# Performance work log

Hardware: AMD Instinct MI355X
Metric: run time of the kernel (lower is better)

## Reference

```python
import jax, jax.numpy as jnp
import numpy as np

B, N, C_IN = 8, 16384, 64
NPOINTS = 1024     # S: number of sampled centers (FPS)
NNEI = 32          # K: neighbors per center (ball query cap)
RADIUS = 0.2
EPS = 1e-5


def fps(pos, S):
    """Farthest point sampling, deterministic start at index 0. pos: [B,N,3] -> [B,S] int32."""
    b, n, _ = pos.shape

    def step(carry, _):
        dist, far = carry
        centroid = jnp.take_along_axis(pos, far[:, None, None], axis=1)  # [B,1,3]
        d = jnp.sum((pos - centroid) ** 2, axis=-1)                       # [B,N]
        dist = jnp.minimum(dist, d)
        return (dist, jnp.argmax(dist, axis=-1).astype(jnp.int32)), far

    init = (jnp.full((b, n), 1e10, pos.dtype), jnp.zeros((b,), jnp.int32))
    _, cent = jax.lax.scan(step, init, None, length=S)  # [S,B]
    return cent.T                                        # [B,S]


def gather(points, idx):
    """points [B,N,C], idx [B,...] -> [B,...,C] (per-batch fancy gather)."""
    return jax.vmap(lambda p, i: p[i])(points, idx)


def ball_query(pos, centers, radius, k):
    """Fixed-radius neighbor search. pos [B,N,3], centers [B,S,3] -> idx [B,S,K] int32.
    Pads short neighborhoods with the first in-radius point (the center itself)."""
    n = pos.shape[1]
    sqr = jnp.sum((centers[:, :, None, :] - pos[:, None, :, :]) ** 2, axis=-1)  # [B,S,N]
    idx = jnp.where(sqr <= radius * radius, jnp.arange(n, dtype=jnp.int32), n)
    idx = jnp.sort(idx, axis=-1)[..., :k]                                        # [B,S,K]
    first = idx[..., :1]
    return jnp.where(idx == n, first, idx)


def conv_bn_relu(x, w, b, g, be):
    """1x1 Conv2d + BatchNorm2d(training stats) + ReLU over grouped tensor x [B,S,K,Cin]."""
    h = jnp.einsum('bskc,cd->bskd', x, w) + b
    mu = jnp.mean(h, axis=(0, 1, 2), keepdims=True)
    var = jnp.mean((h - mu) ** 2, axis=(0, 1, 2), keepdims=True)
    h = (h - mu) * jax.lax.rsqrt(var + EPS) * g + be
    return jax.nn.relu(h)


def reference(pos, feat,
              w_sem1, b_sem1, g_sem1, be_sem1, w_sem2, b_sem2, g_sem2, be_sem2,
              w_geo1, b_geo1, g_geo1, be_geo1, w_geo2, b_geo2, g_geo2, be_geo2):
    centroids = fps(pos, NPOINTS)                       # [B,S]
    centers = gather(pos, centroids)                    # [B,S,3]
    idx = ball_query(pos, centers, RADIUS, NNEI)        # [B,S,K]

    grouped_pos = gather(pos, idx)                      # [B,S,K,3]
    grouped_feat = gather(feat, idx)                    # [B,S,K,C]
    center_rep = jnp.broadcast_to(centers[:, :, None, :], grouped_pos.shape)
    geo_in = jnp.concatenate([center_rep, grouped_pos], axis=-1)  # [B,S,K,6]

    h = conv_bn_relu(grouped_feat, w_sem1, b_sem1, g_sem1, be_sem1)
    h = conv_bn_relu(h, w_sem2, b_sem2, g_sem2, be_sem2)
    h_sem = jnp.max(h, axis=2)                          # [B,S,Cout] max-pool over neighbors

    hg = conv_bn_relu(geo_in, w_geo1, b_geo1, g_geo1, be_geo1)
    hg = conv_bn_relu(hg, w_geo2, b_geo2, g_geo2, be_geo2)
    h_geo = jnp.max(hg, axis=2)                         # [B,S,Cout]

    # original concatenates semantic and geo node features along dim 0
    return jnp.concatenate([h_sem, h_geo], axis=0)      # [2B,S,Cout]


def setup_inputs() -> dict:
    key = jax.random.key(0)
    ks = jax.random.split(key, 12)
    d = {
        'pos': jax.random.uniform(ks[0], (B, N, 3), jnp.float32),
        'feat': jax.random.normal(ks[1], (B, N, C_IN), jnp.float32),
        'w_sem1': jax.random.normal(ks[2], (64, 64), jnp.float32) * 0.05,
        'b_sem1': jnp.zeros((64,), jnp.float32),
        'g_sem1': jnp.ones((64,), jnp.float32),
        'be_sem1': jnp.zeros((64,), jnp.float32),
        'w_sem2': jax.random.normal(ks[3], (64, 128), jnp.float32) * 0.05,
        'b_sem2': jnp.zeros((128,), jnp.float32),
        'g_sem2': jnp.ones((128,), jnp.float32),
        'be_sem2': jnp.zeros((128,), jnp.float32),
        'w_geo1': jax.random.normal(ks[4], (6, 64), jnp.float32) * 0.05,
        'b_geo1': jnp.zeros((64,), jnp.float32),
        'g_geo1': jnp.ones((64,), jnp.float32),
        'be_geo1': jnp.zeros((64,), jnp.float32),
        'w_geo2': jax.random.normal(ks[5], (64, 128), jnp.float32) * 0.05,
        'b_geo2': jnp.zeros((128,), jnp.float32),
        'g_geo2': jnp.ones((128,), jnp.float32),
        'be_geo2': jnp.zeros((128,), jnp.float32),
    }
    return d
```

## Files before the change

### kernel.cpp

```cpp
#include <hip/hip_runtime.h>

#define NB 8
#define NPTS 16384
#define S 1024
#define KNEI 32
#define MROWS (NB*S*KNEI)

typedef float v2f __attribute__((ext_vector_type(2)));

#define DPP_MAXF0(CTRL, v) do {                                               \
    int _o = __builtin_amdgcn_update_dpp(0, __float_as_int(v),                \
                                         (CTRL), 0xF, 0xF, true);             \
    (v) = fmaxf((v), __int_as_float(_o));                                     \
  } while (0)

#define DPP_MINI(CTRL, v) do {                                                \
    int _o = __builtin_amdgcn_update_dpp((int)0x7fffffff, (v),                \
                                         (CTRL), 0xF, 0xF, false);            \
    (v) = (_o < (v)) ? _o : (v);                                              \
  } while (0)

#define DPP_MAXK0(CTRL, k) do {                                               \
    int _olo = __builtin_amdgcn_update_dpp(0, (int)(unsigned)(k),             \
                                           (CTRL), 0xF, 0xF, true);           \
    int _ohi = __builtin_amdgcn_update_dpp(0, (int)(unsigned)((k) >> 32),     \
                                           (CTRL), 0xF, 0xF, true);           \
    unsigned long long _ok = (((unsigned long long)(unsigned)_ohi) << 32)     \
                           | (unsigned)_olo;                                  \
    if (_ok > (k)) (k) = _ok;                                                 \
  } while (0)

#define DPP_ROW_SHR1   0x111
#define DPP_ROW_SHR2   0x112
#define DPP_ROW_SHR4   0x114
#define DPP_ROW_SHR8   0x118
#define DPP_ROW_BCAST15 0x142
#define DPP_ROW_BCAST31 0x143

__global__ __launch_bounds__(1024, 4) void fps_kernel(const float* __restrict__ pos,
                                                      float* __restrict__ centers,
                                                      float* __restrict__ sbuf){
#pragma clang fp contract(off)
  __shared__ int hist[4096];
  __shared__ int ts[1024];
  __shared__ unsigned short perm[16384];
  __shared__ unsigned long long lslotK[2][16];
  const int b = blockIdx.x;
  const int t = threadIdx.x;
  const int wid = t >> 6, lane = t & 63;
  const float* pb = pos + (size_t)b * NPTS * 3;
  float* ssx = sbuf + (size_t)b * 3 * NPTS;
  float* ssy = ssx + NPTS;
  float* ssz = ssy + NPTS;
  const int p0 = t * 16;

  float c[48];
  {
    const float4* src = (const float4*)(pb + (size_t)t*48);
#pragma unroll
    for (int q = 0; q < 12; ++q) *(float4*)&c[q*4] = src[q];
  }
  int cell[16];
#pragma unroll
  for (int j = 0; j < 16; ++j){
    float x = c[3*j], y = c[3*j+1], z = c[3*j+2];
    int ix = (int)(x * 16.f); ix = ix < 0 ? 0 : (ix > 15 ? 15 : ix);
    int iy = (int)(y * 16.f); iy = iy < 0 ? 0 : (iy > 15 ? 15 : iy);
    int iz = (int)(z * 16.f); iz = iz < 0 ? 0 : (iz > 15 ? 15 : iz);
    int m = 0;
#pragma unroll
    for (int k = 0; k < 4; ++k){
      m |= ((ix >> k) & 1) << (3*k + 2);
      m |= ((iy >> k) & 1) << (3*k + 1);
      m |= ((iz >> k) & 1) << (3*k + 0);
    }
    cell[j] = m;
  }
#pragma unroll
  for (int i = 0; i < 4; ++i) hist[t*4 + i] = 0;
  __syncthreads();
#pragma unroll
  for (int j = 0; j < 16; ++j) atomicAdd(&hist[cell[j]], 1);
  __syncthreads();
  int h0 = hist[t*4], h1 = hist[t*4+1], h2v = hist[t*4+2];
  ts[t] = h0 + h1 + h2v + hist[t*4+3];
  __syncthreads();
  for (int off = 1; off < 1024; off <<= 1){
    int add = (t >= off) ? ts[t - off] : 0;
    __syncthreads();
    ts[t] += add;
    __syncthreads();
  }
  {
    int base = (t == 0) ? 0 : ts[t-1];
    hist[t*4]   = base;
    hist[t*4+1] = base + h0;
    hist[t*4+2] = base + h0 + h1;
    hist[t*4+3] = base + h0 + h1 + h2v;
  }
  __syncthreads();
#pragma unroll
  for (int j = 0; j < 16; ++j){
    int dst = atomicAdd(&hist[cell[j]], 1);
    ssx[dst] = c[3*j];
    ssy[dst] = c[3*j+1];
    ssz[dst] = c[3*j+2];
    perm[dst] = (unsigned short)(p0 + j);
  }
  __syncthreads();

  v2f px[8], py[8], pz[8], dist[8];
  int perm_reg[8];
#pragma unroll
  for (int g = 0; g < 4; ++g){
    float4 vx = *(const float4*)&ssx[p0 + g*4];
    float4 vy = *(const float4*)&ssy[p0 + g*4];
    float4 vz = *(const float4*)&ssz[p0 + g*4];
    px[g*2]   = (v2f){vx.x, vx.y}; px[g*2+1] = (v2f){vx.z, vx.w};
    py[g*2]   = (v2f){vy.x, vy.y}; py[g*2+1] = (v2f){vy.z, vy.w};
    pz[g*2]   = (v2f){vz.x, vz.y}; pz[g*2+1] = (v2f){vz.z, vz.w};
  }
#pragma unroll
  for (int j = 0; j < 8; ++j){
    perm_reg[j] = (int)perm[p0 + 2*j] | ((int)perm[p0 + 2*j + 1] << 16);
  }
  float bxl = 1e30f, bxh = -1e30f, byl = 1e30f, byh = -1e30f;
  float bzl = 1e30f, bzh = -1e30f;
#pragma unroll
  for (int j = 0; j < 8; ++j){
    asm volatile("" : "+v"(px[j]), "+v"(py[j]), "+v"(pz[j]), "+v"(perm_reg[j]));
    bxl = fminf(bxl, fminf(px[j].x, px[j].y));
    bxh = fmaxf(bxh, fmaxf(px[j].x, px[j].y));
    byl = fminf(byl, fminf(py[j].x, py[j].y));
    byh = fmaxf(byh, fmaxf(py[j].x, py[j].y));
    bzl = fminf(bzl, fminf(pz[j].x, pz[j].y));
    bzh = fmaxf(bzh, fmaxf(pz[j].x, pz[j].y));
    dist[j] = (v2f){1e10f, 1e10f};
  }
  float ub = 1e10f;
  unsigned long long key = 0;
  float cx = pb[0], cy = pb[1], cz = pb[2];

  for (int s = 0; s < S; ++s){
    if (t == 0){
      float* cd = centers + (size_t)(b*S + s)*3;
      cd[0] = cx; cd[1] = cy; cd[2] = cz;
    }
    float lx = fmaxf(fmaxf(bxl - cx, cx - bxh), 0.f);
    float ly = fmaxf(fmaxf(byl - cy, cy - byh), 0.f);
    float lz = fmaxf(fmaxf(bzl - cz, cz - bzh), 0.f);
    float lb2 = ((lx*lx + ly*ly) + lz*lz);
    bool act = !(lb2 * 0.99999f >= ub);
    unsigned long long am = __ballot((int)act);
    if (am){
      if (act){
        v2f cx2 = (v2f){cx, cx}, cy2 = (v2f){cy, cy}, cz2 = (v2f){cz, cz};
        float nb = 0.0f;
#pragma unroll
        for (int j = 0; j < 8; ++j){
          v2f dx = px[j] - cx2;
          v2f dy = py[j] - cy2;
          v2f dz = pz[j] - cz2;
          v2f t1 = dx * dx;
          v2f t2 = dy * dy;
          v2f t3 = dz * dz;
          v2f d  = (t1 + t2) + t3;
          v2f od = dist[j];
          v2f nd = (v2f){__builtin_fminf(od.x, d.x), __builtin_fminf(od.y, d.y)};
          dist[j] = nd;
          nb = fmaxf(fmaxf(nb, nd.x), nd.y);
        }
        ub = nb;
      }
      float bv = ub;
      DPP_MAXF0(DPP_ROW_SHR1,   bv);
      DPP_MAXF0(DPP_ROW_SHR2,   bv);
      DPP_MAXF0(DPP_ROW_SHR4,   bv);
      DPP_MAXF0(DPP_ROW_SHR8,   bv);
      DPP_MAXF0(DPP_ROW_BCAST15, bv);
      DPP_MAXF0(DPP_ROW_BCAST31, bv);
      float bmw = __int_as_float(
          __builtin_amdgcn_readlane(__float_as_int(bv), 63));
      int mi = 0x7fffffff;
      if (ub == bmw){
#pragma unroll
        for (int j = 0; j < 8; ++j){
          if (dist[j].x == bmw){ int o = perm_reg[j] & 0xffff;         mi = o < mi ? o : mi; }
          if (dist[j].y == bmw){ int o = (perm_reg[j] >> 16) & 0xffff; mi = o < mi ? o : mi; }
        }
      }
      DPP_MINI(DPP_ROW_SHR1,   mi);
      DPP_MINI(DPP_ROW_SHR2,   mi);
      DPP_MINI(DPP_ROW_SHR4,   mi);
      DPP_MINI(DPP_ROW_SHR8,   mi);
      DPP_MINI(DPP_ROW_BCAST15, mi);
      DPP_MINI(DPP_ROW_BCAST31, mi);
      int miw = __builtin_amdgcn_readlane(mi, 63);
      key = ((unsigned long long)__float_as_uint(bmw) << 15)
          | (unsigned long long)(16384 - miw);
    }
    const int par = s & 1;
    if (lane == 0) lslotK[par][wid] = key;
    __syncthreads();
    unsigned long long kk = lslotK[par][lane & 15];
    DPP_MAXK0(DPP_ROW_SHR1, kk);
    DPP_MAXK0(DPP_ROW_SHR2, kk);
    DPP_MAXK0(DPP_ROW_SHR4, kk);
    DPP_MAXK0(DPP_ROW_SHR8, kk);
    unsigned blo = (unsigned)__builtin_amdgcn_readlane((int)(unsigned)kk, 15);
    unsigned bhi = (unsigned)__builtin_amdgcn_readlane((int)(unsigned)(kk >> 32), 15);
    unsigned long long kmax = (((unsigned long long)bhi) << 32) | blo;
    int ufi = 16384 - (int)(kmax & 0x7FFFull);
    const float* cp = pb + (size_t)ufi*3;
    cx = cp[0]; cy = cp[1]; cz = cp[2];
  }
}

__global__ __launch_bounds__(256) void ballq_kernel(const float* __restrict__ pos,
                                                    const float* __restrict__ centers,
                                                    int* __restrict__ idx){
#pragma clang fp contract(off)
  const float R2 = (float)(0.2*0.2);
  int wid  = blockIdx.x*4 + (threadIdx.x >> 6);
  int lane = threadIdx.x & 63;
  int b = wid >> 10;
  const float* pb = pos + (size_t)b * NPTS * 3;
  float cx = centers[wid*3+0], cy = centers[wid*3+1], cz = centers[wid*3+2];
  int* out = idx + wid*KNEI;
  int count = 0; int first = -1;
  for (int base = 0; base < NPTS; base += 64){
    int p = base + lane;
    float dx = pb[p*3+0]-cx, dy = pb[p*3+1]-cy, dz = pb[p*3+2]-cz;
    float t1 = dx*dx, t2 = dy*dy, t3 = dz*dz;
    float d = (t1 + t2) + t3;
    bool inr = d <= R2;
    unsigned long long mask = __ballot(inr);
    if (count == 0 && mask) first = base + __builtin_ctzll(mask);
    if (inr){
      int slot = count + __popcll(mask & ((1ull << lane) - 1ull));
      if (slot < KNEI) out[slot] = p;
    }
    count += __popcll(mask);
    if (count >= KNEI) break;
  }
  if (count < KNEI){
    for (int slot = count + lane; slot < KNEI; slot += 64) out[slot] = first;
  }
}

__global__ __launch_bounds__(256) void gemm_sem1(const float* __restrict__ feat,
    const int* __restrict__ idx, const float* __restrict__ w,
    const float* __restrict__ bias, float* __restrict__ h1,
    float* __restrict__ stat){
  __shared__ float xs[64][68];
  __shared__ float wsh[64][64];
  const int tid = threadIdx.x;
  const int m0 = blockIdx.x * 64;
#pragma unroll
  for (int i = 0; i < 4; ++i){
    int q = tid + i*256;
    int r = q >> 4, c4 = q & 15;
    *(float4*)&wsh[r][c4*4] = *(const float4*)&w[r*64 + c4*4];
  }
#pragma unroll
  for (int i = 0; i < 4; ++i){
    int q = tid + i*256;
    int r = q >> 4, c4 = q & 15;
    int m = m0 + r;
    int nb = idx[m];
    int b = m >> 15;
    const float* fr = feat + ((size_t)b*NPTS + nb)*64;
    *(float4*)&xs[r][c4*4] = *(const float4*)&fr[c4*4];
  }
  __syncthreads();
  const int g  = tid & 7;
  const int rt = tid >> 3;
  const int r0 = rt * 2;
  float acc[2][8];
#pragma unroll
  for (int c = 0; c < 8; ++c){ float bb = bias[g*8+c]; acc[0][c] = bb; acc[1][c] = bb; }
  for (int k = 0; k < 64; ++k){
    float x0 = xs[r0][k], x1 = xs[r0+1][k];
    float4 wa = *(float4*)&wsh[k][g*8];
    float4 wb = *(float4*)&wsh[k][g*8+4];
    float wv[8] = {wa.x,wa.y,wa.z,wa.w,wb.x,wb.y,wb.z,wb.w};
#pragma unroll
    for (int c = 0; c < 8; ++c){ acc[0][c] += x0*wv[c]; acc[1][c] += x1*wv[c]; }
  }
#pragma unroll
  for (int r = 0; r < 2; ++r){
    float* dst = h1 + (size_t)(m0 + r0 + r)*64 + g*8;
    *(float4*)dst     = make_float4(acc[r][0],acc[r][1],acc[r][2],acc[r][3]);
    *(float4*)(dst+4) = make_float4(acc[r][4],acc[r][5],acc[r][6],acc[r][7]);
  }
  float ls[8], lq[8];
#pragma unroll
  for (int c = 0; c < 8; ++c){
    ls[c] = acc[0][c] + acc[1][c];
    lq[c] = acc[0][c]*acc[0][c] + acc[1][c]*acc[1][c];
  }
  __syncthreads();
  float* red  = &xs[0][0];
  float* redq = &wsh[0][0];
#pragma unroll
  for (int c = 0; c < 8; ++c){
    red[(g*8+c)*32 + rt]  = ls[c];
    redq[(g*8+c)*32 + rt] = lq[c];
  }
  __syncthreads();
  if (tid < 128){
    int c = tid & 63;
    const float* src = (tid < 64) ? red : redq;
    float a2 = 0.f;
    for (int i = 0; i < 32; ++i) a2 += src[c*32+i];
    atomicAdd(&stat[(tid < 64 ? 0 : 64) + c], a2);
  }
}

__global__ __launch_bounds__(256) void gemm2_fused(const float* __restrict__ hin,
    const float* __restrict__ abn, const float* __restrict__ dbn,
    const float* __restrict__ w, const float* __restrict__ bias,
    float* __restrict__ hmax, float* __restrict__ stat){
  __shared__ float xs[64][68];
  __shared__ float wsh[64][128];
  const int tid = threadIdx.x;
  const int m0 = blockIdx.x * 64;
#pragma unroll
  for (int i = 0; i < 8; ++i){
    int q = tid + i*256;
    int r = q >> 5, c4 = q & 31;
    *(float4*)&wsh[r][c4*4] = *(const float4*)&w[r*128 + c4*4];
  }
#pragma unroll
  for (int i = 0; i < 4; ++i){
    int q = tid + i*256;
    int r = q >> 4, c4 = q & 15;
    float4 v  = *(const float4*)&hin[(size_t)(m0+r)*64 + c4*4];
    float4 av = *(const float4*)&abn[c4*4];
    float4 dv = *(const float4*)&dbn[c4*4];
    v.x = fmaxf(v.x*av.x + dv.x, 0.f);
    v.y = fmaxf(v.y*av.y + dv.y, 0.f);
    v.z = fmaxf(v.z*av.z + dv.z, 0.f);
    v.w = fmaxf(v.w*av.w + dv.w, 0.f);
    *(float4*)&xs[r][c4*4] = v;
  }
  __syncthreads();
  const int g  = tid & 15;
  const int rt = tid >> 4;
  const int r0 = rt * 4;
  float acc[4][8];
#pragma unroll
  for (int c = 0; c < 8; ++c){
    float bb = bias[g*8+c];
    acc[0][c]=bb; acc[1][c]=bb; acc[2][c]=bb; acc[3][c]=bb;
  }
  for (int k = 0; k < 64; ++k){
    float x0 = xs[r0][k], x1 = xs[r0+1][k], x2 = xs[r0+2][k], x3 = xs[r0+3][k];
    float4 wa = *(float4*)&wsh[k][g*8];
    float4 wb = *(float4*)&wsh[k][g*8+4];
    float wv[8] = {wa.x,wa.y,wa.z,wa.w,wb.x,wb.y,wb.z,wb.w};
#pragma unroll
    for (int c = 0; c < 8; ++c){
      acc[0][c] += x0*wv[c]; acc[1][c] += x1*wv[c];
      acc[2][c] += x2*wv[c]; acc[3][c] += x3*wv[c];
    }
  }
  float ls[8], lq[8], tmax[8];
#pragma unroll
  for (int c = 0; c < 8; ++c){
    ls[c] = acc[0][c]+acc[1][c]+acc[2][c]+acc[3][c];
    lq[c] = acc[0][c]*acc[0][c]+acc[1][c]*acc[1][c]+acc[2][c]*acc[2][c]+acc[3][c]*acc[3][c];
    tmax[c] = fmaxf(fmaxf(acc[0][c],acc[1][c]), fmaxf(acc[2][c],acc[3][c]));
  }
  __syncthreads();
  float* red  = &xs[0][0];
  float* mred = &wsh[0][0];
#pragma unroll
  for (int c = 0; c < 8; ++c){
    red[(g*8+c)*16 + rt]        = ls[c];
    red[2048 + (g*8+c)*16 + rt] = lq[c];
    mred[rt*128 + g*8 + c]      = tmax[c];
  }
  __syncthreads();
  {
    int c = tid & 127;
    int isq = tid >> 7;
    float a2 = 0.f;
    for (int i = 0; i < 16; ++i) a2 += red[isq*2048 + c*16 + i];
    atomicAdd(&stat[isq*128 + c], a2);
  }
  {
    int og = tid >> 7;
    int c  = tid & 127;
    float m = -3.4e38f;
#pragma unroll
    for (int i = 0; i < 8; ++i) m = fmaxf(m, mred[(og*8 + i)*128 + c]);
    hmax[(size_t)(blockIdx.x*2 + og)*128 + c] = m;
  }
}

__global__ __launch_bounds__(256) void gemm_geo1(const float* __restrict__ pos,
    const float* __restrict__ centers, const int* __restrict__ idx,
    const float* __restrict__ w, const float* __restrict__ bias,
    float* __restrict__ hout, float* __restrict__ stat){
  __shared__ float xs[64][8];
  __shared__ float wsh[6][64];
  __shared__ float red[2048];
  __shared__ float redq[2048];
  const int tid = threadIdx.x;
  const int m0 = blockIdx.x * 64;
  for (int i = tid; i < 384; i += 256) wsh[i >> 6][i & 63] = w[i];
  if (tid < 64){
    int m = m0 + tid;
    int grp = m >> 5;
    int b = m >> 15;
    int nb = idx[m];
    const float* cp = centers + (size_t)grp*3;
    const float* pp = pos + ((size_t)b*NPTS + nb)*3;
    xs[tid][0]=cp[0]; xs[tid][1]=cp[1]; xs[tid][2]=cp[2];
    xs[tid][3]=pp[0]; xs[tid][4]=pp[1]; xs[tid][5]=pp[2];
  }
  __syncthreads();
  const int g  = tid & 7;
  const int rt = tid >> 3;
  const int r0 = rt * 2;
  float acc[2][8];
#pragma unroll
  for (int c = 0; c < 8; ++c){ float bb = bias[g*8+c]; acc[0][c]=bb; acc[1][c]=bb; }
#pragma unroll
  for (int k = 0; k < 6; ++k){
    float x0 = xs[r0][k], x1 = xs[r0+1][k];
    float4 wa = *(float4*)&wsh[k][g*8];
    float4 wb = *(float4*)&wsh[k][g*8+4];
    float wv[8] = {wa.x,wa.y,wa.z,wa.w,wb.x,wb.y,wb.z,wb.w};
#pragma unroll
    for (int c = 0; c < 8; ++c){ acc[0][c] += x0*wv[c]; acc[1][c] += x1*wv[c]; }
  }
#pragma unroll
  for (int r = 0; r < 2; ++r){
    float* dst = hout + (size_t)(m0 + r0 + r)*64 + g*8;
    *(float4*)dst     = make_float4(acc[r][0],acc[r][1],acc[r][2],acc[r][3]);
    *(float4*)(dst+4) = make_float4(acc[r][4],acc[r][5],acc[r][6],acc[r][7]);
  }
  float ls[8], lq[8];
#pragma unroll
  for (int c = 0; c < 8; ++c){
    ls[c] = acc[0][c] + acc[1][c];
    lq[c] = acc[0][c]*acc[0][c] + acc[1][c]*acc[1][c];
  }
#pragma unroll
  for (int c = 0; c < 8; ++c){
    red[(g*8+c)*32 + rt]  = ls[c];
    redq[(g*8+c)*32 + rt] = lq[c];
  }
  __syncthreads();
  if (tid < 128){
    int c = tid & 63;
    const float* src = (tid < 64) ? red : redq;
    float a2 = 0.f;
    for (int i = 0; i < 32; ++i) a2 += src[c*32+i];
    atomicAdd(&stat[(tid < 64 ? 0 : 64) + c], a2);
  }
}

__global__ void bn_finalize(const float* __restrict__ stat,
                            const float* __restrict__ gam, const float* __restrict__ bet,
                            float* __restrict__ a, float* __restrict__ d, int C){
  int c = threadIdx.x;
  if (c >= C) return;
  const float invM = 1.0f / (float)MROWS;
  float mu  = stat[c] * invM;
  float ex2 = stat[C + c] * invM;
  float var = ex2 - mu*mu;
  float aa = gam[c] * rsqrtf(var + 1e-5f);
  a[c] = aa;
  d[c] = bet[c] - mu*aa;
}

__global__ __launch_bounds__(256) void bnapply_kernel(const float* __restrict__ hmax,
    const float* __restrict__ abn, const float* __restrict__ dbn,
    float* __restrict__ out){
  int i = blockIdx.x*256 + threadIdx.x;
  int c = i & 127;
  out[i] = fmaxf(hmax[i]*abn[c] + dbn[c], 0.f);
}

__global__ void zero_kernel(float* __restrict__ p, int n){
  int i = blockIdx.x*blockDim.x + threadIdx.x;
  if (i < n) p[i] = 0.f;
}

extern "C" void kernel_launch(void* const* d_in, const int* in_sizes, int n_in,
                              void* d_out, int out_size, void* d_ws, size_t ws_size,
                              hipStream_t stream){
  const float* pos   = (const float*)d_in[0];
  const float* feat  = (const float*)d_in[1];
  const float* w_s1  = (const float*)d_in[2];
  const float* b_s1  = (const float*)d_in[3];
  const float* g_s1  = (const float*)d_in[4];
  const float* be_s1 = (const float*)d_in[5];
  const float* w_s2  = (const float*)d_in[6];
  const float* b_s2  = (const float*)d_in[7];
  const float* g_s2  = (const float*)d_in[8];
  const float* be_s2 = (const float*)d_in[9];
  const float* w_g1  = (const float*)d_in[10];
  const float* b_g1  = (const float*)d_in[11];
  const float* g_g1  = (const float*)d_in[12];
  const float* be_g1 = (const float*)d_in[13];
  const float* w_g2  = (const float*)d_in[14];
  const float* b_g2  = (const float*)d_in[15];
  const float* g_g2  = (const float*)d_in[16];
  const float* be_g2 = (const float*)d_in[17];
  float* outp = (float*)d_out;
  float* wsf  = (float*)d_ws;

  float* centers = wsf;
  int*   idxp    = (int*)(wsf + 24576);
  float* stats   = wsf + 24576 + 262144;
  float* bnad    = stats + 768;
  float* h1      = wsf + 288256;
  float* scratch = h1 + (size_t)MROWS*64;
  float* sortbuf = scratch;
  float* hmax1   = scratch + 524288;
  float* hmax2   = scratch + 524288 + 1048576;

  float* st1 = stats;
  float* st2 = stats + 128;
  float* st3 = stats + 384;
  float* st4 = stats + 512;
  float* a1 = bnad;        float* d1 = bnad + 64;
  float* a2 = bnad + 128;  float* d2 = bnad + 256;
  float* a3 = bnad + 384;  float* d3 = bnad + 448;
  float* a4 = bnad + 512;  float* d4 = bnad + 640;

  zero_kernel<<<3, 256, 0, stream>>>(stats, 768);
  fps_kernel<<<NB, 1024, 0, stream>>>(pos, centers, sortbuf);
  ballq_kernel<<<(NB*S)/4, 256, 0, stream>>>(pos, centers, idxp);

  gemm_sem1<<<MROWS/64, 256, 0, stream>>>(feat, idxp, w_s1, b_s1, h1, st1);
  bn_finalize<<<1, 128, 0, stream>>>(st1, g_s1, be_s1, a1, d1, 64);
  gemm2_fused<<<MROWS/64, 256, 0, stream>>>(h1, a1, d1, w_s2, b_s2, hmax1, st2);
  bn_finalize<<<1, 128, 0, stream>>>(st2, g_s2, be_s2, a2, d2, 128);
  bnapply_kernel<<<(NB*S*128)/256, 256, 0, stream>>>(hmax1, a2, d2, outp);

  gemm_geo1<<<MROWS/64, 256, 0, stream>>>(pos, centers, idxp, w_g1, b_g1, h1, st3);
  bn_finalize<<<1, 128, 0, stream>>>(st3, g_g1, be_g1, a3, d3, 64);
  gemm2_fused<<<MROWS/64, 256, 0, stream>>>(h1, a3, d3, w_g2, b_g2, hmax2, st4);
  bn_finalize<<<1, 128, 0, stream>>>(st4, g_g2, be_g2, a4, d4, 128);
  bnapply_kernel<<<(NB*S*128)/256, 256, 0, stream>>>(hmax2, a4, d4, outp + (size_t)NB*S*128);
}
```

Before: 1.712 ms.

## Merge sem/geo branch kernels, fold stats zeroing, broadcast FPS winner via readlane

The semantic and geometric MLP branches now run in shared launches: one combined layer-1 GEMM, one combined layer-2 GEMM, batched BN finalize and a single BN-apply kernel. This removes about half the kernel launches and serialization gaps, and gives each launch a larger grid. Zeroing the stats buffer moves into the ball-query kernel, which drops the separate zero kernel. In FPS, each of the 16 candidate lanes preloads its point's coordinates before the reduction, and the winner's coordinates are taken with a ballot plus readlane instead of a dependent global load after the argmax. The cost is a second h1 buffer in workspace and a wasted coordinate load on every FPS iteration.

```diff
diff --git a/kernel.cpp b/kernel.cpp
--- a/kernel.cpp
+++ b/kernel.cpp
@@ -203,23 +203,31 @@
     if (lane == 0) lslotK[par][wid] = key;
     __syncthreads();
     unsigned long long kk = lslotK[par][lane & 15];
+    int ufi_l = 16384 - (int)(kk & 0x7FFFull);
+    const float* cpl = pb + (size_t)ufi_l*3;
+    float wx = cpl[0], wy = cpl[1], wz = cpl[2];
+    unsigned long long kko = kk;
     DPP_MAXK0(DPP_ROW_SHR1, kk);
     DPP_MAXK0(DPP_ROW_SHR2, kk);
     DPP_MAXK0(DPP_ROW_SHR4, kk);
     DPP_MAXK0(DPP_ROW_SHR8, kk);
     unsigned blo = (unsigned)__builtin_amdgcn_readlane((int)(unsigned)kk, 15);
     unsigned bhi = (unsigned)__builtin_amdgcn_readlane((int)(unsigned)(kk >> 32), 15);
-    unsigned long long kmax = (((unsigned long long)bhi) << 32) | blo;
-    int ufi = 16384 - (int)(kmax & 0x7FFFull);
-    const float* cp = pb + (size_t)ufi*3;
-    cx = cp[0]; cy = cp[1]; cz = cp[2];
+    unsigned long long bkmax = (((unsigned long long)bhi) << 32) | blo;
+    unsigned m16 = (unsigned)__ballot((int)(kko == bkmax)) & 0xffffu;
+    int sidx = (int)__builtin_ctz(m16);
+    cx = __int_as_float(__builtin_amdgcn_readlane(__float_as_int(wx), sidx));
+    cy = __int_as_float(__builtin_amdgcn_readlane(__float_as_int(wy), sidx));
+    cz = __int_as_float(__builtin_amdgcn_readlane(__float_as_int(wz), sidx));
   }
 }
 
 __global__ __launch_bounds__(256) void ballq_kernel(const float* __restrict__ pos,
                                                     const float* __restrict__ centers,
-                                                    int* __restrict__ idx){
+                                                    int* __restrict__ idx,
+                                                    float* __restrict__ stats){
 #pragma clang fp contract(off)
+  if (blockIdx.x < 3) stats[blockIdx.x*256 + threadIdx.x] = 0.f;
   const float R2 = (float)(0.2*0.2);
   int wid  = blockIdx.x*4 + (threadIdx.x >> 6);
   int lane = threadIdx.x & 63;
@@ -248,83 +256,161 @@
   }
 }
 
-__global__ __launch_bounds__(256) void gemm_sem1(const float* __restrict__ feat,
-    const int* __restrict__ idx, const float* __restrict__ w,
-    const float* __restrict__ bias, float* __restrict__ h1,
-    float* __restrict__ stat){
-  __shared__ float xs[64][68];
-  __shared__ float wsh[64][64];
+__global__ __launch_bounds__(256) void gemm1_both(const float* __restrict__ feat,
+    const float* __restrict__ pos, const float* __restrict__ centers,
+    const int* __restrict__ idx,
+    const float* __restrict__ w_s, const float* __restrict__ b_s,
+    float* __restrict__ h1s, float* __restrict__ st_s,
+    const float* __restrict__ w_g, const float* __restrict__ b_g,
+    float* __restrict__ h1g, float* __restrict__ st_g){
+  __shared__ float smem[8448];
   const int tid = threadIdx.x;
-  const int m0 = blockIdx.x * 64;
-#pragma unroll
-  for (int i = 0; i < 4; ++i){
-    int q = tid + i*256;
-    int r = q >> 4, c4 = q & 15;
-    *(float4*)&wsh[r][c4*4] = *(const float4*)&w[r*64 + c4*4];
-  }
-#pragma unroll
-  for (int i = 0; i < 4; ++i){
-    int q = tid + i*256;
-    int r = q >> 4, c4 = q & 15;
-    int m = m0 + r;
-    int nb = idx[m];
-    int b = m >> 15;
-    const float* fr = feat + ((size_t)b*NPTS + nb)*64;
-    *(float4*)&xs[r][c4*4] = *(const float4*)&fr[c4*4];
-  }
-  __syncthreads();
-  const int g  = tid & 7;
-  const int rt = tid >> 3;
-  const int r0 = rt * 2;
-  float acc[2][8];
-#pragma unroll
-  for (int c = 0; c < 8; ++c){ float bb = bias[g*8+c]; acc[0][c] = bb; acc[1][c] = bb; }
-  for (int k = 0; k < 64; ++k){
-    float x0 = xs[r0][k], x1 = xs[r0+1][k];
-    float4 wa = *(float4*)&wsh[k][g*8];
-    float4 wb = *(float4*)&wsh[k][g*8+4];
-    float wv[8] = {wa.x,wa.y,wa.z,wa.w,wb.x,wb.y,wb.z,wb.w};
-#pragma unroll
-    for (int c = 0; c < 8; ++c){ acc[0][c] += x0*wv[c]; acc[1][c] += x1*wv[c]; }
-  }
-#pragma unroll
-  for (int r = 0; r < 2; ++r){
-    float* dst = h1 + (size_t)(m0 + r0 + r)*64 + g*8;
-    *(float4*)dst     = make_float4(acc[r][0],acc[r][1],acc[r][2],acc[r][3]);
-    *(float4*)(dst+4) = make_float4(acc[r][4],acc[r][5],acc[r][6],acc[r][7]);
-  }
-  float ls[8], lq[8];
-#pragma unroll
-  for (int c = 0; c < 8; ++c){
-    ls[c] = acc[0][c] + acc[1][c];
-    lq[c] = acc[0][c]*acc[0][c] + acc[1][c]*acc[1][c];
-  }
-  __syncthreads();
-  float* red  = &xs[0][0];
-  float* redq = &wsh[0][0];
-#pragma unroll
-  for (int c = 0; c < 8; ++c){
-    red[(g*8+c)*32 + rt]  = ls[c];
-    redq[(g*8+c)*32 + rt] = lq[c];
-  }
-  __syncthreads();
-  if (tid < 128){
-    int c = tid & 63;
-    const float* src = (tid < 64) ? red : redq;
-    float a2 = 0.f;
-    for (int i = 0; i < 32; ++i) a2 += src[c*32+i];
-    atomicAdd(&stat[(tid < 64 ? 0 : 64) + c], a2);
-  }
-}
-
-__global__ __launch_bounds__(256) void gemm2_fused(const float* __restrict__ hin,
-    const float* __restrict__ abn, const float* __restrict__ dbn,
-    const float* __restrict__ w, const float* __restrict__ bias,
-    float* __restrict__ hmax, float* __restrict__ stat){
+  if (blockIdx.x < (MROWS/64)){
+    float (*xs)[68]  = (float(*)[68])smem;
+    float (*wsh)[64] = (float(*)[64])(smem + 4352);
+    const int m0 = blockIdx.x * 64;
+#pragma unroll
+    for (int i = 0; i < 4; ++i){
+      int q = tid + i*256;
+      int r = q >> 4, c4 = q & 15;
+      *(float4*)&wsh[r][c4*4] = *(const float4*)&w_s[r*64 + c4*4];
+    }
+#pragma unroll
+    for (int i = 0; i < 4; ++i){
+      int q = tid + i*256;
+      int r = q >> 4, c4 = q & 15;
+      int m = m0 + r;
+      int nb = idx[m];
+      int b = m >> 15;
+      const float* fr = feat + ((size_t)b*NPTS + nb)*64;
+      *(float4*)&xs[r][c4*4] = *(const float4*)&fr[c4*4];
+    }
+    __syncthreads();
+    const int g  = tid & 7;
+    const int rt = tid >> 3;
+    const int r0 = rt * 2;
+    float acc[2][8];
+#pragma unroll
+    for (int c = 0; c < 8; ++c){ float bb = b_s[g*8+c]; acc[0][c] = bb; acc[1][c] = bb; }
+    for (int k = 0; k < 64; ++k){
+      float x0 = xs[r0][k], x1 = xs[r0+1][k];
+      float4 wa = *(float4*)&wsh[k][g*8];
+      float4 wb = *(float4*)&wsh[k][g*8+4];
+      float wv[8] = {wa.x,wa.y,wa.z,wa.w,wb.x,wb.y,wb.z,wb.w};
+#pragma unroll
+      for (int c = 0; c < 8; ++c){ acc[0][c] += x0*wv[c]; acc[1][c] += x1*wv[c]; }
+    }
+#pragma unroll
+    for (int r = 0; r < 2; ++r){
+      float* dst = h1s + (size_t)(m0 + r0 + r)*64 + g*8;
+      *(float4*)dst     = make_float4(acc[r][0],acc[r][1],acc[r][2],acc[r][3]);
+      *(float4*)(dst+4) = make_float4(acc[r][4],acc[r][5],acc[r][6],acc[r][7]);
+    }
+    float ls[8], lq[8];
+#pragma unroll
+    for (int c = 0; c < 8; ++c){
+      ls[c] = acc[0][c] + acc[1][c];
+      lq[c] = acc[0][c]*acc[0][c] + acc[1][c]*acc[1][c];
+    }
+    __syncthreads();
+    float* red  = smem;
+    float* redq = smem + 4352;
+#pragma unroll
+    for (int c = 0; c < 8; ++c){
+      red[(g*8+c)*32 + rt]  = ls[c];
+      redq[(g*8+c)*32 + rt] = lq[c];
+    }
+    __syncthreads();
+    if (tid < 128){
+      int c = tid & 63;
+      const float* src = (tid < 64) ? red : redq;
+      float a2 = 0.f;
+      for (int i = 0; i < 32; ++i) a2 += src[c*32+i];
+      atomicAdd(&st_s[(tid < 64 ? 0 : 64) + c], a2);
+    }
+  } else {
+    float (*xs)[8]   = (float(*)[8])smem;
+    float (*wsh)[64] = (float(*)[64])(smem + 512);
+    float* red  = smem + 896;
+    float* redq = smem + 2944;
+    const int m0 = (blockIdx.x - (MROWS/64)) * 64;
+    for (int i = tid; i < 384; i += 256) wsh[i >> 6][i & 63] = w_g[i];
+    if (tid < 64){
+      int m = m0 + tid;
+      int grp = m >> 5;
+      int b = m >> 15;
+      int nb = idx[m];
+      const float* cp = centers + (size_t)grp*3;
+      const float* pp = pos + ((size_t)b*NPTS + nb)*3;
+      xs[tid][0]=cp[0]; xs[tid][1]=cp[1]; xs[tid][2]=cp[2];
+      xs[tid][3]=pp[0]; xs[tid][4]=pp[1]; xs[tid][5]=pp[2];
+    }
+    __syncthreads();
+    const int g  = tid & 7;
+    const int rt = tid >> 3;
+    const int r0 = rt * 2;
+    float acc[2][8];
+#pragma unroll
+    for (int c = 0; c < 8; ++c){ float bb = b_g[g*8+c]; acc[0][c]=bb; acc[1][c]=bb; }
+#pragma unroll
+    for (int k = 0; k < 6; ++k){
+      float x0 = xs[r0][k], x1 = xs[r0+1][k];
+      float4 wa = *(float4*)&wsh[k][g*8];
+      float4 wb = *(float4*)&wsh[k][g*8+4];
+      float wv[8] = {wa.x,wa.y,wa.z,wa.w,wb.x,wb.y,wb.z,wb.w};
+#pragma unroll
+      for (int c = 0; c < 8; ++c){ acc[0][c] += x0*wv[c]; acc[1][c] += x1*wv[c]; }
+    }
+#pragma unroll
+    for (int r = 0; r < 2; ++r){
+      float* dst = h1g + (size_t)(m0 + r0 + r)*64 + g*8;
+      *(float4*)dst     = make_float4(acc[r][0],acc[r][1],acc[r][2],acc[r][3]);
+      *(float4*)(dst+4) = make_float4(acc[r][4],acc[r][5],acc[r][6],acc[r][7]);
+    }
+    float ls[8], lq[8];
+#pragma unroll
+    for (int c = 0; c < 8; ++c){
+      ls[c] = acc[0][c] + acc[1][c];
+      lq[c] = acc[0][c]*acc[0][c] + acc[1][c]*acc[1][c];
+    }
+#pragma unroll
+    for (int c = 0; c < 8; ++c){
+      red[(g*8+c)*32 + rt]  = ls[c];
+      redq[(g*8+c)*32 + rt] = lq[c];
+    }
+    __syncthreads();
+    if (tid < 128){
+      int c = tid & 63;
+      const float* src = (tid < 64) ? red : redq;
+      float a2 = 0.f;
+      for (int i = 0; i < 32; ++i) a2 += src[c*32+i];
+      atomicAdd(&st_g[(tid < 64 ? 0 : 64) + c], a2);
+    }
+  }
+}
+
+__global__ __launch_bounds__(256) void gemm2_both(
+    const float* __restrict__ h1s, const float* __restrict__ a1,
+    const float* __restrict__ d1, const float* __restrict__ w_s2,
+    const float* __restrict__ b_s2, float* __restrict__ hmax1,
+    float* __restrict__ st2,
+    const float* __restrict__ h1g, const float* __restrict__ a3,
+    const float* __restrict__ d3, const float* __restrict__ w_g2,
+    const float* __restrict__ b_g2, float* __restrict__ hmax2,
+    float* __restrict__ st4){
   __shared__ float xs[64][68];
   __shared__ float wsh[64][128];
   const int tid = threadIdx.x;
-  const int m0 = blockIdx.x * 64;
+  const bool sem = blockIdx.x < (MROWS/64);
+  const int bx = sem ? blockIdx.x : blockIdx.x - (MROWS/64);
+  const float* hin  = sem ? h1s  : h1g;
+  const float* abn  = sem ? a1   : a3;
+  const float* dbn  = sem ? d1   : d3;
+  const float* w    = sem ? w_s2 : w_g2;
+  const float* bias = sem ? b_s2 : b_g2;
+  float* hmax       = sem ? hmax1 : hmax2;
+  float* stat       = sem ? st2  : st4;
+  const int m0 = bx * 64;
 #pragma unroll
   for (int i = 0; i < 8; ++i){
     int q = tid + i*256;
@@ -395,79 +481,23 @@
     float m = -3.4e38f;
 #pragma unroll
     for (int i = 0; i < 8; ++i) m = fmaxf(m, mred[(og*8 + i)*128 + c]);
-    hmax[(size_t)(blockIdx.x*2 + og)*128 + c] = m;
-  }
-}
-
-__global__ __launch_bounds__(256) void gemm_geo1(const float* __restrict__ pos,
-    const float* __restrict__ centers, const int* __restrict__ idx,
-    const float* __restrict__ w, const float* __restrict__ bias,
-    float* __restrict__ hout, float* __restrict__ stat){
-  __shared__ float xs[64][8];
-  __shared__ float wsh[6][64];
-  __shared__ float red[2048];
-  __shared__ float redq[2048];
-  const int tid = threadIdx.x;
-  const int m0 = blockIdx.x * 64;
-  for (int i = tid; i < 384; i += 256) wsh[i >> 6][i & 63] = w[i];
-  if (tid < 64){
-    int m = m0 + tid;
-    int grp = m >> 5;
-    int b = m >> 15;
-    int nb = idx[m];
-    const float* cp = centers + (size_t)grp*3;
-    const float* pp = pos + ((size_t)b*NPTS + nb)*3;
-    xs[tid][0]=cp[0]; xs[tid][1]=cp[1]; xs[tid][2]=cp[2];
-    xs[tid][3]=pp[0]; xs[tid][4]=pp[1]; xs[tid][5]=pp[2];
-  }
-  __syncthreads();
-  const int g  = tid & 7;
-  const int rt = tid >> 3;
-  const int r0 = rt * 2;
-  float acc[2][8];
-#pragma unroll
-  for (int c = 0; c < 8; ++c){ float bb = bias[g*8+c]; acc[0][c]=bb; acc[1][c]=bb; }
-#pragma unroll
-  for (int k = 0; k < 6; ++k){
-    float x0 = xs[r0][k], x1 = xs[r0+1][k];
-    float4 wa = *(float4*)&wsh[k][g*8];
-    float4 wb = *(float4*)&wsh[k][g*8+4];
-    float wv[8] = {wa.x,wa.y,wa.z,wa.w,wb.x,wb.y,wb.z,wb.w};
-#pragma unroll
-    for (int c = 0; c < 8; ++c){ acc[0][c] += x0*wv[c]; acc[1][c] += x1*wv[c]; }
-  }
-#pragma unroll
-  for (int r = 0; r < 2; ++r){
-    float* dst = hout + (size_t)(m0 + r0 + r)*64 + g*8;
-    *(float4*)dst     = make_float4(acc[r][0],acc[r][1],acc[r][2],acc[r][3]);
-    *(float4*)(dst+4) = make_float4(acc[r][4],acc[r][5],acc[r][6],acc[r][7]);
-  }
-  float ls[8], lq[8];
-#pragma unroll
-  for (int c = 0; c < 8; ++c){
-    ls[c] = acc[0][c] + acc[1][c];
-    lq[c] = acc[0][c]*acc[0][c] + acc[1][c]*acc[1][c];
-  }
-#pragma unroll
-  for (int c = 0; c < 8; ++c){
-    red[(g*8+c)*32 + rt]  = ls[c];
-    redq[(g*8+c)*32 + rt] = lq[c];
-  }
-  __syncthreads();
-  if (tid < 128){
-    int c = tid & 63;
-    const float* src = (tid < 64) ? red : redq;
-    float a2 = 0.f;
-    for (int i = 0; i < 32; ++i) a2 += src[c*32+i];
-    atomicAdd(&stat[(tid < 64 ? 0 : 64) + c], a2);
-  }
-}
-
-__global__ void bn_finalize(const float* __restrict__ stat,
-                            const float* __restrict__ gam, const float* __restrict__ bet,
-                            float* __restrict__ a, float* __restrict__ d, int C){
+    hmax[(size_t)(bx*2 + og)*128 + c] = m;
+  }
+}
+
+__global__ void bn_finalize2(const float* __restrict__ stA,
+    const float* __restrict__ gamA, const float* __restrict__ betA,
+    float* __restrict__ aA, float* __restrict__ dA,
+    const float* __restrict__ stB,
+    const float* __restrict__ gamB, const float* __restrict__ betB,
+    float* __restrict__ aB, float* __restrict__ dB, int C){
   int c = threadIdx.x;
   if (c >= C) return;
+  const float* stat = blockIdx.x ? stB : stA;
+  const float* gam  = blockIdx.x ? gamB : gamA;
+  const float* bet  = blockIdx.x ? betB : betA;
+  float* a = blockIdx.x ? aB : aA;
+  float* d = blockIdx.x ? dB : dA;
   const float invM = 1.0f / (float)MROWS;
   float mu  = stat[c] * invM;
   float ex2 = stat[C + c] * invM;
@@ -477,17 +507,21 @@
   d[c] = bet[c] - mu*aa;
 }
 
-__global__ __launch_bounds__(256) void bnapply_kernel(const float* __restrict__ hmax,
-    const float* __restrict__ abn, const float* __restrict__ dbn,
+__global__ __launch_bounds__(256) void bnapply_both(const float* __restrict__ hmax1,
+    const float* __restrict__ a2, const float* __restrict__ d2,
+    const float* __restrict__ hmax2,
+    const float* __restrict__ a4, const float* __restrict__ d4,
     float* __restrict__ out){
+  const int half = NB*S*128;
   int i = blockIdx.x*256 + threadIdx.x;
-  int c = i & 127;
-  out[i] = fmaxf(hmax[i]*abn[c] + dbn[c], 0.f);
-}
-
-__global__ void zero_kernel(float* __restrict__ p, int n){
-  int i = blockIdx.x*blockDim.x + threadIdx.x;
-  if (i < n) p[i] = 0.f;
+  if (i < half){
+    int c = i & 127;
+    out[i] = fmaxf(hmax1[i]*a2[c] + d2[c], 0.f);
+  } else {
+    int j = i - half;
+    int c = j & 127;
+    out[i] = fmaxf(hmax2[j]*a4[c] + d4[c], 0.f);
+  }
 }
 
 extern "C" void kernel_launch(void* const* d_in, const int* in_sizes, int n_in,
@@ -518,11 +552,11 @@
   int*   idxp    = (int*)(wsf + 24576);
   float* stats   = wsf + 24576 + 262144;
   float* bnad    = stats + 768;
-  float* h1      = wsf + 288256;
-  float* scratch = h1 + (size_t)MROWS*64;
-  float* sortbuf = scratch;
-  float* hmax1   = scratch + 524288;
-  float* hmax2   = scratch + 524288 + 1048576;
+  float* h1s     = wsf + 288256;
+  float* h1g     = h1s + (size_t)MROWS*64;
+  float* sortbuf = h1g + (size_t)MROWS*64;
+  float* hmax1   = sortbuf + 393216;
+  float* hmax2   = hmax1 + 1048576;
 
   float* st1 = stats;
   float* st2 = stats + 128;
@@ -533,19 +567,16 @@
   float* a3 = bnad + 384;  float* d3 = bnad + 448;
   float* a4 = bnad + 512;  float* d4 = bnad + 640;
 
-  zero_kernel<<<3, 256, 0, stream>>>(stats, 768);
   fps_kernel<<<NB, 1024, 0, stream>>>(pos, centers, sortbuf);
-  ballq_kernel<<<(NB*S)/4, 256, 0, stream>>>(pos, centers, idxp);
-
-  gemm_sem1<<<MROWS/64, 256, 0, stream>>>(feat, idxp, w_s1, b_s1, h1, st1);
-  bn_finalize<<<1, 128, 0, stream>>>(st1, g_s1, be_s1, a1, d1, 64);
-  gemm2_fused<<<MROWS/64, 256, 0, stream>>>(h1, a1, d1, w_s2, b_s2, hmax1, st2);
-  bn_finalize<<<1, 128, 0, stream>>>(st2, g_s2, be_s2, a2, d2, 128);
-  bnapply_kernel<<<(NB*S*128)/256, 256, 0, stream>>>(hmax1, a2, d2, outp);
-
-  gemm_geo1<<<MROWS/64, 256, 0, stream>>>(pos, centers, idxp, w_g1, b_g1, h1, st3);
-  bn_finalize<<<1, 128, 0, stream>>>(st3, g_g1, be_g1, a3, d3, 64);
-  gemm2_fused<<<MROWS/64, 256, 0, stream>>>(h1, a3, d3, w_g2, b_g2, hmax2, st4);
-  bn_finalize<<<1, 128, 0, stream>>>(st4, g_g2, be_g2, a4, d4, 128);
-  bnapply_kernel<<<(NB*S*128)/256, 256, 0, stream>>>(hmax2, a4, d4, outp + (size_t)NB*S*128);
-}
+  ballq_kernel<<<(NB*S)/4, 256, 0, stream>>>(pos, centers, idxp, stats);
+  gemm1_both<<<2*(MROWS/64), 256, 0, stream>>>(feat, pos, centers, idxp,
+      w_s1, b_s1, h1s, st1, w_g1, b_g1, h1g, st3);
+  bn_finalize2<<<2, 128, 0, stream>>>(st1, g_s1, be_s1, a1, d1,
+                                      st3, g_g1, be_g1, a3, d3, 64);
+  gemm2_both<<<2*(MROWS/64), 256, 0, stream>>>(h1s, a1, d1, w_s2, b_s2, hmax1, st2,
+                                               h1g, a3, d3, w_g2, b_g2, hmax2, st4);
+  bn_finalize2<<<2, 128, 0, stream>>>(st2, g_s2, be_s2, a2, d2,
+                                      st4, g_g2, be_g2, a4, d4, 128);
+  bnapply_both<<<(2*NB*S*128)/256, 256, 0, stream>>>(hmax1, a2, d2,
+                                                     hmax2, a4, d4, outp);
+}
```

After: 1.661 ms. -3.0%, faster.
